# Kernel optimization log

Hardware: AMD Instinct MI355X
Metric: run time of the kernel (lower is better)

The kernel has to match this reference:

```python
import jax, jax.numpy as jnp
import numpy as np

B = 65536
NE = 256   # n_encode
NH = 256   # n_hidden
NC = 4     # n_command
D = 64     # n_depth (BatchNorm channels)
F = 32     # n_features
M = D * (F // 2)  # 1024
EPS = 1e-5


def setup_inputs() -> dict:
    key = jax.random.key(0)
    ks = jax.random.split(key, 8)
    s = 0.05
    return {
        "feature": jax.random.normal(ks[0], (B, NE), jnp.float32),
        "hidden":  jax.random.normal(ks[1], (B, NH), jnp.float32),
        "command": jax.random.normal(ks[2], (B, NC), jnp.float32),
        # linear weights (torch Linear stores [out, in]); xavier-like scale
        "Wq":  jax.random.normal(ks[3], (D, NC), jnp.float32) * s,
        "Wkz": jax.random.normal(ks[4], (M, NE), jnp.float32) * s,
        "Wkh": jax.random.normal(ks[5], (M, NH), jnp.float32) * s,
        "Wvz": jax.random.normal(ks[6], (M, NE), jnp.float32) * s,
        "Wvh": jax.random.normal(ks[7], (M, NH), jnp.float32) * s,
        # BatchNorm1d(64) affine params (normV exists in __init__ but is unused)
        "gammaQ": jnp.ones((D,), jnp.float32),
        "betaQ":  jnp.zeros((D,), jnp.float32),
        "gammaK": jnp.ones((D,), jnp.float32),
        "betaK":  jnp.zeros((D,), jnp.float32),
    }


def reference(feature, hidden, command, Wq, Wkz, Wkh, Wvz, Wvh,
              gammaQ, betaQ, gammaK, betaK):
    # Q projection: [B, D]; BatchNorm1d over batch (training-mode batch stats,
    # biased variance, matching torch).
    Q = command @ Wq.T
    mQ = jnp.mean(Q, axis=0)
    vQ = jnp.mean(jnp.square(Q - mQ), axis=0)
    Qn = (Q - mQ) / jnp.sqrt(vQ + EPS) * gammaQ + betaQ          # [B, D]

    # K: cat([B,M],[B,M]) -> [B, 2M] -> view [B, F, D] -> transpose -> [B, D, F]
    K = jnp.concatenate([feature @ Wkz.T, hidden @ Wkh.T], axis=1)
    K = K.reshape(-1, F, D).transpose(0, 2, 1)                    # [B, D, F]
    mK = jnp.mean(K, axis=(0, 2), keepdims=True)
    vK = jnp.mean(jnp.square(K - mK), axis=(0, 2), keepdims=True)
    Kn = (K - mK) / jnp.sqrt(vK + EPS) * gammaK[None, :, None] + betaK[None, :, None]

    # V: [B, F, D], NOT batch-normed (normV is dead code in the original)
    V = jnp.concatenate([feature @ Wvz.T, hidden @ Wvh.T], axis=1).reshape(-1, F, D)

    # attention: [B,1,D] @ [B,D,F] -> [B,F] scores; softmax over F; then @ V
    A = jax.nn.softmax(jnp.einsum('bd,bdf->bf', Qn, Kn) / np.sqrt(D).astype(np.float32), axis=-1)
    s = jnp.einsum('bf,bfd->bd', A, V)                            # [B, D]
    return s
```

## Files before the change

kernel.cpp:

```cpp
#include <hip/hip_runtime.h>
#include <hip/hip_bf16.h>
#include <math.h>


typedef float  f32x4   __attribute__((ext_vector_type(4)));
typedef float  f32x16  __attribute__((ext_vector_type(16)));
typedef __bf16 bf16x4  __attribute__((ext_vector_type(4)));
typedef __bf16 bf16x8  __attribute__((ext_vector_type(8)));

#define MFMA16(A, B, C) __builtin_amdgcn_mfma_f32_16x16x32_bf16((A), (B), (C), 0, 0, 0)
#define MFMA32(A, B, C) __builtin_amdgcn_mfma_f32_32x32x16_bf16((A), (B), (C), 0, 0, 0)

#define EPSV 1e-5f

#define WS_WV    0x000000u
#define WS_WKF   0x100000u
#define WS_G     0x120000u
#define WS_CS    0x1A0000u
#define WS_CMDP  0x1A0800u
#define WS_T     0x1A1800u
#define WS_U     0x1A3800u
#define WS_WQ2   0x1A5800u
#define WS_C0    0x1A5C00u

__global__ __launch_bounds__(512, 2) void setup1(const float* __restrict__ feat,
        const float* __restrict__ hid, const float4* __restrict__ cmd,
        const float* __restrict__ Wvz, const float* __restrict__ Wvh,
        __bf16* __restrict__ WV, float* __restrict__ CMDP, float* __restrict__ CS,
        __bf16* __restrict__ Gp)
{
    __shared__ __bf16 T[256 * 40];
    __shared__ float sm[8][14];
    const int blk = blockIdx.x;
    const int tid = threadIdx.x;

    if (blk >= 384) {
        const int b2 = blk - 384;
        float v[14];
#pragma unroll
        for (int k = 0; k < 14; ++k) v[k] = 0.f;
#pragma unroll
        for (int i = 0; i < 4; ++i) {
            float4 c = cmd[(b2 * 4 + i) * 512 + tid];
            v[0] += c.x;  v[1] += c.y;  v[2] += c.z;  v[3] += c.w;
            v[4] += c.x*c.x; v[5] += c.x*c.y; v[6] += c.x*c.z; v[7] += c.x*c.w;
            v[8] += c.y*c.y; v[9] += c.y*c.z; v[10] += c.y*c.w;
            v[11] += c.z*c.z; v[12] += c.z*c.w; v[13] += c.w*c.w;
        }
#pragma unroll
        for (int k = 0; k < 14; ++k) {
            float s = v[k];
#pragma unroll
            for (int off = 32; off; off >>= 1) s += __shfl_xor(s, off);
            if ((tid & 63) == 0) sm[tid >> 6][k] = s;
        }
        __syncthreads();
        if (tid < 14) {
            float s = 0.f;
#pragma unroll
            for (int w = 0; w < 8; ++w) s += sm[w][tid];
            CMDP[b2 * 14 + tid] = s;
        }
        return;
    }
    if (blk >= 128) {
        int t = (blk - 128) * 512 + tid;
        int e = t * 4;
        const float* src = (e < 262144) ? (Wvz + e) : (Wvh + (e - 262144));
        float4 a = *(const float4*)src;
        bf16x4 vv = { (__bf16)a.x, (__bf16)a.y, (__bf16)a.z, (__bf16)a.w };
        *(bf16x4*)(WV + e) = vv;
        return;
    }

    const int mat  = blk >> 6;
    const int chunk = blk & 63;
    const float* X = mat ? hid : feat;
    float* cs = CS + mat * 256;
    const int k0   = chunk * 1024;
    const int wid  = tid >> 6, lane = tid & 63, quad = lane >> 4, l15 = lane & 15;
    const int c    = tid & 255;
    const int t8   = tid >> 8;

    f32x4 acc[2][16];
#pragma unroll
    for (int mt = 0; mt < 2; ++mt)
#pragma unroll
        for (int nt = 0; nt < 16; ++nt) acc[mt][nt] = (f32x4){0.f, 0.f, 0.f, 0.f};

    float clsum = 0.f;
    for (int it = 0; it < 32; ++it) {
        __syncthreads();
        const int kb = k0 + it * 32;
#pragma unroll
        for (int i = 0; i < 16; ++i) {
            int k = t8 + 2 * i;
            float x = X[(size_t)(kb + k) * 256 + c];
            clsum += x;
            T[c * 40 + k] = (__bf16)x;
        }
        __syncthreads();
        bf16x8 a0 = *(const bf16x8*)&T[(wid * 32 +      l15) * 40 + quad * 8];
        bf16x8 a1 = *(const bf16x8*)&T[(wid * 32 + 16 + l15) * 40 + quad * 8];
#pragma unroll
        for (int nt = 0; nt < 16; ++nt) {
            bf16x8 b = *(const bf16x8*)&T[(nt * 16 + l15) * 40 + quad * 8];
            acc[0][nt] = MFMA16(a0, b, acc[0][nt]);
            acc[1][nt] = MFMA16(a1, b, acc[1][nt]);
        }
    }
    atomicAdd(&cs[c], clsum);
    __bf16* outp = Gp + (size_t)blk * 65536;
#pragma unroll
    for (int mt = 0; mt < 2; ++mt)
#pragma unroll
        for (int nt = 0; nt < 16; ++nt)
#pragma unroll
            for (int r = 0; r < 4; ++r) {
                int gi = wid * 32 + mt * 16 + quad * 4 + r;
                int gj = nt * 16 + l15;
                outp[gi * 256 + gj] = (__bf16)acc[mt][nt][r];
            }
}

__global__ void gram_reduce(const __bf16* __restrict__ Gp, float* __restrict__ G)
{
    int o = blockIdx.x * 256 + threadIdx.x;
    int mat = o >> 16, e = o & 65535;
    const __bf16* p = Gp + (size_t)mat * 64 * 65536 + e;
    float s = 0.f;
#pragma unroll 8
    for (int c = 0; c < 64; ++c) s += (float)p[(size_t)c * 65536];
    G[o] = s;
}

__global__ void rowstats(const float* __restrict__ Wkz, const float* __restrict__ Wkh,
        const float* __restrict__ G, const float* __restrict__ CS,
        float* __restrict__ Tout, float* __restrict__ Uout)
{
    const int blk = blockIdx.x;
    const int mat = blk >> 7, jg = blk & 127;
    const float* Wsrc = (mat ? Wkh : Wkz) + (size_t)jg * 8 * 256;
    const float* Gm = G + (size_t)mat * 65536;
    const float* cs = CS + mat * 256;
    __shared__ float wlT[256 * 8];
    __shared__ float red[4][16];
    const int tid = threadIdx.x, wid = tid >> 6, lane = tid & 63;
#pragma unroll
    for (int jj = 0; jj < 8; ++jj) wlT[tid * 8 + jj] = Wsrc[jj * 256 + tid];
    __syncthreads();
    float inner[8];
#pragma unroll
    for (int jj = 0; jj < 8; ++jj) inner[jj] = 0.f;
    for (int r = 0; r < 256; ++r) {
        float g = Gm[r * 256 + tid];
        float4 w0 = *(const float4*)&wlT[r * 8];
        float4 w1 = *(const float4*)&wlT[r * 8 + 4];
        inner[0] = fmaf(w0.x, g, inner[0]); inner[1] = fmaf(w0.y, g, inner[1]);
        inner[2] = fmaf(w0.z, g, inner[2]); inner[3] = fmaf(w0.w, g, inner[3]);
        inner[4] = fmaf(w1.x, g, inner[4]); inner[5] = fmaf(w1.y, g, inner[5]);
        inner[6] = fmaf(w1.z, g, inner[6]); inner[7] = fmaf(w1.w, g, inner[7]);
    }
    float cst = cs[tid];
#pragma unroll
    for (int jj = 0; jj < 8; ++jj) {
        float wme = wlT[tid * 8 + jj];
        float p = wme * inner[jj];
        float u = wme * cst;
#pragma unroll
        for (int off = 32; off; off >>= 1) { p += __shfl_xor(p, off); u += __shfl_xor(u, off); }
        if (lane == 0) { red[wid][jj] = p; red[wid][jj + 8] = u; }
    }
    __syncthreads();
    if (tid < 16) {
        float s = red[0][tid] + red[1][tid] + red[2][tid] + red[3][tid];
        int jj = tid & 7;
        int j = mat * 1024 + jg * 8 + jj;
        if (tid < 8) Tout[j] = s; else Uout[j] = s;
    }
}

__global__ void finalize_kernel(const float* __restrict__ Wq,
        const float* __restrict__ gQ, const float* __restrict__ bQ,
        const float* __restrict__ gK, const float* __restrict__ bK,
        const float* __restrict__ CMDP, const float* __restrict__ T,
        const float* __restrict__ U, float* __restrict__ Wq2, float* __restrict__ C0)
{
    __shared__ float s14[14];
    const int d = threadIdx.x;
    if (d < 14) {
        float s = 0.f;
        for (int b = 0; b < 32; ++b) s += CMDP[b * 14 + d];
        s14[d] = s;
    }
    __syncthreads();
    float s4[4] = { s14[0], s14[1], s14[2], s14[3] };
    float gc[4][4];
    gc[0][0] = s14[4];
    gc[0][1] = gc[1][0] = s14[5];
    gc[0][2] = gc[2][0] = s14[6];
    gc[0][3] = gc[3][0] = s14[7];
    gc[1][1] = s14[8];
    gc[1][2] = gc[2][1] = s14[9];
    gc[1][3] = gc[3][1] = s14[10];
    gc[2][2] = s14[11];
    gc[2][3] = gc[3][2] = s14[12];
    gc[3][3] = s14[13];
    float wq[4];
#pragma unroll
    for (int c = 0; c < 4; ++c) wq[c] = Wq[d * 4 + c];
    const float invB = 1.0f / 65536.0f;
    float mQ = (wq[0]*s4[0] + wq[1]*s4[1] + wq[2]*s4[2] + wq[3]*s4[3]) * invB;
    float eq2 = 0.f;
#pragma unroll
    for (int c = 0; c < 4; ++c)
#pragma unroll
        for (int c2 = 0; c2 < 4; ++c2) eq2 += wq[c] * wq[c2] * gc[c][c2];
    eq2 *= invB;
    float vQ  = eq2 - mQ * mQ;
    float aQ  = gQ[d] / sqrtf(vQ + EPSV);
    float bQv = bQ[d] - mQ * aQ;
    float S2 = 0.f, S1 = 0.f;
#pragma unroll
    for (int f = 0; f < 32; ++f) { S2 += T[f * 64 + d]; S1 += U[f * 64 + d]; }
    const float invBF = 1.0f / (65536.0f * 32.0f);
    float e2 = S2 * invBF, mK = S1 * invBF;
    float vK = e2 - mK * mK;
    float aK = gK[d] / sqrtf(vK + EPSV);
    float c1 = aQ * aK * 0.125f;
    C0[d] = bQv * aK * 0.125f;
#pragma unroll
    for (int c = 0; c < 4; ++c) Wq2[d * 4 + c] = c1 * wq[c];
}

__global__ void foldK(const float* __restrict__ Wkz, const float* __restrict__ Wkh,
                      const float* __restrict__ Wq2, const float* __restrict__ C0,
                      __bf16* __restrict__ WKF)
{
    const int blk = blockIdx.x;
    const int h = blk / 96, rr = blk % 96;
    const int k = threadIdx.x;
    float s = 0.f;
    if (rr < 80) {
        const int c = rr >> 4, fl = rr & 15;
        const float* Wsrc = (h ? Wkh : Wkz) + (size_t)fl * 64 * 256;
        for (int d = 0; d < 64; ++d) {
            float coef = (c == 0) ? C0[d] : Wq2[d * 4 + (c - 1)];
            s = fmaf(coef, Wsrc[d * 256 + k], s);
        }
    }
    WKF[(size_t)(h * 96 + rr) * 256 + k] = (__bf16)s;
}

__global__ __launch_bounds__(256, 2) void fused_attn(
        const float* __restrict__ feat, const float* __restrict__ hid,
        const float4* __restrict__ cmd, const __bf16* __restrict__ WV,
        const __bf16* __restrict__ WKF, float* __restrict__ out)
{
    __shared__ __bf16 BUF[32768];
    __shared__ __bf16 WGTs[16 * 128];
    const int tid  = threadIdx.x;
    const int wid  = tid >> 6, lane = tid & 63;
    const int l5   = lane & 31, hi = lane >> 5;
    const int fl   = l5 & 15;
    const bool low = (l5 < 16);
    const int wrow = (blockIdx.x << 7) + (wid << 5);

    float l_i[16];
    f32x16 s_acc[2];
#pragma unroll
    for (int r = 0; r < 16; ++r) { l_i[r] = 0.f; s_acc[0][r] = 0.f; s_acc[1][r] = 0.f; }

    bf16x8 st[8];

    for (int h = 0; h < 2; ++h) {
        const float* X = h ? hid : feat;
        const __bf16* Wkf = WKF + ((size_t)h * 96 << 8);

        bf16x8 a2[16];
#pragma unroll
        for (int u = 0; u < 16; ++u) {
            const float* p = X + ((size_t)(wrow + l5) << 8) + u * 16 + hi * 8;
            float4 x0 = *(const float4*)p;
            float4 x1 = *(const float4*)(p + 4);
            a2[u] = (bf16x8){ (__bf16)x0.x, (__bf16)x0.y, (__bf16)x0.z, (__bf16)x0.w,
                              (__bf16)x1.x, (__bf16)x1.y, (__bf16)x1.z, (__bf16)x1.w };
        }

        __syncthreads();
#pragma unroll
        for (int i = 0; i < 12; ++i) {
            int cc = tid + i * 256;
            int n = cc >> 5, k8 = cc & 31;
            bf16x8 v = *(const bf16x8*)(Wkf + n * 256 + k8 * 8);
            *(bf16x8*)&BUF[n * 256 + ((k8 ^ (n & 7)) << 3)] = v;
        }
        __syncthreads();

        f32x16 acc1[3];
#pragma unroll
        for (int nt = 0; nt < 3; ++nt)
#pragma unroll
            for (int r = 0; r < 16; ++r) acc1[nt][r] = 0.f;
#pragma unroll
        for (int ks = 0; ks < 16; ++ks)
#pragma unroll
            for (int nt = 0; nt < 3; ++nt) {
                int n = nt * 32 + l5;
                bf16x8 b = *(const bf16x8*)&BUF[n * 256 + (((ks * 2 + hi) ^ (n & 7)) << 3)];
                acc1[nt] = MFMA32(a2[ks], b, acc1[nt]);
            }

#pragma unroll
        for (int g = 0; g < 4; ++g) {
            bf16x4 wv4;
#pragma unroll
            for (int j = 0; j < 4; ++j) {
                const int r = g * 4 + j;
                const int row32 = j + 8 * g + 4 * hi;
                float4 cm = cmd[wrow + row32];
                float e0, e1, t0[3], t1[3];
#pragma unroll
                for (int nt = 0; nt < 3; ++nt) {
                    e0 = acc1[nt][r];
                    e1 = __shfl_xor(e0, 16);
                    t0[nt] = low ? e0 : e1;
                    t1[nt] = low ? e1 : e0;
                }
                float sc = t0[0] + cm.x * t1[0] + cm.y * t0[1]
                                 + cm.z * t1[1] + cm.w * t0[2];
                float w = __expf(sc);
                wv4[j] = (__bf16)w;
                float ws = w;
                ws += __shfl_xor(ws, 1); ws += __shfl_xor(ws, 2);
                ws += __shfl_xor(ws, 4); ws += __shfl_xor(ws, 8);
                l_i[r] += ws;
            }
            if (low) *(bf16x4*)&WGTs[fl * 128 + (wid << 5) + 8 * g + 4 * hi] = wv4;
        }

        if (h == 0) {
            const __bf16* base = WV;
#pragma unroll
            for (int i = 0; i < 8; ++i) {
                int cc = tid + i * 256;
                int n = cc >> 5, k8 = cc & 31;
                st[i] = *(const bf16x8*)(base + n * 256 + k8 * 8);
            }
        }
        __syncthreads();

        for (int f2 = 0; f2 < 16; ++f2) {
            const int bufsel = (f2 & 1) << 14;
#pragma unroll
            for (int i = 0; i < 8; ++i) {
                int cc = tid + i * 256;
                int n = cc >> 5, k8 = cc & 31;
                *(bf16x8*)&BUF[bufsel + n * 256 + ((k8 ^ (n & 7)) << 3)] = st[i];
            }
            __syncthreads();
            const int g2 = h * 16 + f2 + 1;
            if (g2 < 32) {
                const __bf16* base = WV + ((size_t)g2 << 14);
#pragma unroll
                for (int i = 0; i < 8; ++i) {
                    int cc = tid + i * 256;
                    int n = cc >> 5, k8 = cc & 31;
                    st[i] = *(const bf16x8*)(base + n * 256 + k8 * 8);
                }
            }
            f32x16 acc2[2];
#pragma unroll
            for (int r = 0; r < 16; ++r) { acc2[0][r] = 0.f; acc2[1][r] = 0.f; }
#pragma unroll
            for (int ks = 0; ks < 16; ++ks)
#pragma unroll
                for (int nt = 0; nt < 2; ++nt) {
                    int n = nt * 32 + l5;
                    bf16x8 b = *(const bf16x8*)&BUF[bufsel + n * 256
                                                    + (((ks * 2 + hi) ^ (n & 7)) << 3)];
                    acc2[nt] = MFMA32(a2[ks], b, acc2[nt]);
                }
#pragma unroll
            for (int g = 0; g < 4; ++g) {
                bf16x4 wv = *(const bf16x4*)&WGTs[f2 * 128 + (wid << 5) + 8 * g + 4 * hi];
#pragma unroll
                for (int j = 0; j < 4; ++j) {
                    float w = (float)wv[j];
                    s_acc[0][g * 4 + j] += w * acc2[0][g * 4 + j];
                    s_acc[1][g * 4 + j] += w * acc2[1][g * 4 + j];
                }
            }
        }
    }

#pragma unroll
    for (int g = 0; g < 4; ++g)
#pragma unroll
        for (int j = 0; j < 4; ++j) {
            const int r = g * 4 + j;
            float inv = 1.0f / l_i[r];
            size_t row = (size_t)(wrow + j + 8 * g + 4 * hi);
            out[(row << 6) + l5]      = s_acc[0][r] * inv;
            out[(row << 6) + 32 + l5] = s_acc[1][r] * inv;
        }
}

extern "C" void kernel_launch(void* const* d_in, const int* in_sizes, int n_in,
                              void* d_out, int out_size, void* d_ws, size_t ws_size,
                              hipStream_t stream)
{
    (void)in_sizes; (void)n_in; (void)out_size; (void)ws_size;
    const float* feature = (const float*)d_in[0];
    const float* hidden  = (const float*)d_in[1];
    const float* command = (const float*)d_in[2];
    const float* Wq      = (const float*)d_in[3];
    const float* Wkz     = (const float*)d_in[4];
    const float* Wkh     = (const float*)d_in[5];
    const float* Wvz     = (const float*)d_in[6];
    const float* Wvh     = (const float*)d_in[7];
    const float* gammaQ  = (const float*)d_in[8];
    const float* betaQ   = (const float*)d_in[9];
    const float* gammaK  = (const float*)d_in[10];
    const float* betaK   = (const float*)d_in[11];

    char* ws = (char*)d_ws;
    __bf16* WV   = (__bf16*)(ws + WS_WV);
    __bf16* WKF  = (__bf16*)(ws + WS_WKF);
    float*  G    = (float*)(ws + WS_G);
    float*  CS   = (float*)(ws + WS_CS);
    float*  CMDP = (float*)(ws + WS_CMDP);
    float*  Tj   = (float*)(ws + WS_T);
    float*  Uj   = (float*)(ws + WS_U);
    float*  Wq2  = (float*)(ws + WS_WQ2);
    float*  C0   = (float*)(ws + WS_C0);
    float*  outp = (float*)d_out;
    __bf16* Gp   = (__bf16*)d_out;

    hipMemsetAsync(ws + WS_CS, 0, 0x800, stream);
    setup1<<<416, 512, 0, stream>>>(feature, hidden, (const float4*)command,
                                    Wvz, Wvh, WV, CMDP, CS, Gp);
    gram_reduce<<<512, 256, 0, stream>>>(Gp, G);
    rowstats<<<256, 256, 0, stream>>>(Wkz, Wkh, G, CS, Tj, Uj);
    finalize_kernel<<<1, 64, 0, stream>>>(Wq, gammaQ, betaQ, gammaK, betaK,
                                          CMDP, Tj, Uj, Wq2, C0);
    foldK<<<192, 256, 0, stream>>>(Wkz, Wkh, Wq2, C0, WKF);
    fused_attn<<<512, 256, 0, stream>>>(feature, hidden, (const float4*)command,
                                        WV, WKF, outp);
}
```

Baseline: 374.0 us.

## Load weight tiles straight into LDS with global_load_lds and raise MFMA priority

The key-weight and value-weight tiles now go from global memory directly into swizzled LDS through the global_load_lds builtin, replacing the register-staged load-then-store path. The value-weight loop keeps two LDS buffers and issues the next tile's asynchronous load right after the barrier, while MFMAs run on the current buffer. This frees the staging VGPRs and removes the LDS store instructions. It also wraps the MFMA loops in s_setprio and adds a sched_barrier. The risk is correctness: it relies on barriers waiting for the DMA loads to finish, and the fixed per-wave lane-to-row mapping must cover every row.

Measured after the change: 360.3 us. 1.04x faster.

```diff
diff --git a/kernel.cpp b/kernel.cpp
--- a/kernel.cpp
+++ b/kernel.cpp
@@ -22,6 +22,13 @@
 #define WS_U     0x1A3800u
 #define WS_WQ2   0x1A5800u
 #define WS_C0    0x1A5C00u
+
+__device__ __forceinline__ void gl_lds16(const void* g, void* l)
+{
+    __builtin_amdgcn_global_load_lds(
+        (const __attribute__((address_space(1))) unsigned int*)g,
+        (__attribute__((address_space(3))) unsigned int*)l, 16, 0, 0);
+}
 
 __global__ __launch_bounds__(512, 2) void setup1(const float* __restrict__ feat,
         const float* __restrict__ hid, const float4* __restrict__ cmd,
@@ -266,12 +273,17 @@
     const bool low = (l5 < 16);
     const int wrow = (blockIdx.x << 7) + (wid << 5);
 
+    int voff[12];
+#pragma unroll
+    for (int i = 0; i < 12; ++i) {
+        int n = (wid << 1) + (i << 3) + hi;
+        voff[i] = n * 256 + ((l5 ^ (n & 7)) << 3);
+    }
+
     float l_i[16];
     f32x16 s_acc[2];
 #pragma unroll
     for (int r = 0; r < 16; ++r) { l_i[r] = 0.f; s_acc[0][r] = 0.f; s_acc[1][r] = 0.f; }
-
-    bf16x8 st[8];
 
     for (int h = 0; h < 2; ++h) {
         const float* X = h ? hid : feat;
@@ -289,12 +301,8 @@
 
         __syncthreads();
 #pragma unroll
-        for (int i = 0; i < 12; ++i) {
-            int cc = tid + i * 256;
-            int n = cc >> 5, k8 = cc & 31;
-            bf16x8 v = *(const bf16x8*)(Wkf + n * 256 + k8 * 8);
-            *(bf16x8*)&BUF[n * 256 + ((k8 ^ (n & 7)) << 3)] = v;
-        }
+        for (int i = 0; i < 12; ++i)
+            gl_lds16(Wkf + voff[i], &BUF[((wid << 1) + (i << 3)) << 8]);
         __syncthreads();
 
         f32x16 acc1[3];
@@ -302,6 +310,7 @@
         for (int nt = 0; nt < 3; ++nt)
 #pragma unroll
             for (int r = 0; r < 16; ++r) acc1[nt][r] = 0.f;
+        __builtin_amdgcn_s_setprio(1);
 #pragma unroll
         for (int ks = 0; ks < 16; ++ks)
 #pragma unroll
@@ -310,6 +319,7 @@
                 bf16x8 b = *(const bf16x8*)&BUF[n * 256 + (((ks * 2 + hi) ^ (n & 7)) << 3)];
                 acc1[nt] = MFMA32(a2[ks], b, acc1[nt]);
             }
+        __builtin_amdgcn_s_setprio(0);
 
 #pragma unroll
         for (int g = 0; g < 4; ++g) {
@@ -339,39 +349,30 @@
             if (low) *(bf16x4*)&WGTs[fl * 128 + (wid << 5) + 8 * g + 4 * hi] = wv4;
         }
 
-        if (h == 0) {
-            const __bf16* base = WV;
-#pragma unroll
-            for (int i = 0; i < 8; ++i) {
-                int cc = tid + i * 256;
-                int n = cc >> 5, k8 = cc & 31;
-                st[i] = *(const bf16x8*)(base + n * 256 + k8 * 8);
-            }
-        }
-        __syncthreads();
+        __syncthreads();
+
+        {
+            const __bf16* base = WV + ((size_t)(h * 16) << 14);
+#pragma unroll
+            for (int i = 0; i < 8; ++i)
+                gl_lds16(base + voff[i], &BUF[((wid << 1) + (i << 3)) << 8]);
+        }
 
         for (int f2 = 0; f2 < 16; ++f2) {
             const int bufsel = (f2 & 1) << 14;
-#pragma unroll
-            for (int i = 0; i < 8; ++i) {
-                int cc = tid + i * 256;
-                int n = cc >> 5, k8 = cc & 31;
-                *(bf16x8*)&BUF[bufsel + n * 256 + ((k8 ^ (n & 7)) << 3)] = st[i];
+            __syncthreads();
+            if (f2 < 15) {
+                const __bf16* base = WV + ((size_t)(h * 16 + f2 + 1) << 14);
+                const int nsel = bufsel ^ 16384;
+#pragma unroll
+                for (int i = 0; i < 8; ++i)
+                    gl_lds16(base + voff[i], &BUF[nsel + ((((wid << 1) + (i << 3))) << 8)]);
             }
-            __syncthreads();
-            const int g2 = h * 16 + f2 + 1;
-            if (g2 < 32) {
-                const __bf16* base = WV + ((size_t)g2 << 14);
-#pragma unroll
-                for (int i = 0; i < 8; ++i) {
-                    int cc = tid + i * 256;
-                    int n = cc >> 5, k8 = cc & 31;
-                    st[i] = *(const bf16x8*)(base + n * 256 + k8 * 8);
-                }
-            }
+            __builtin_amdgcn_sched_barrier(0);
             f32x16 acc2[2];
 #pragma unroll
             for (int r = 0; r < 16; ++r) { acc2[0][r] = 0.f; acc2[1][r] = 0.f; }
+            __builtin_amdgcn_s_setprio(1);
 #pragma unroll
             for (int ks = 0; ks < 16; ++ks)
 #pragma unroll
@@ -381,6 +382,7 @@
                                                     + (((ks * 2 + hi) ^ (n & 7)) << 3)];
                     acc2[nt] = MFMA32(a2[ks], b, acc2[nt]);
                 }
+            __builtin_amdgcn_s_setprio(0);
 #pragma unroll
             for (int g = 0; g < 4; ++g) {
                 bf16x4 wv = *(const bf16x4*)&WGTs[f2 * 128 + (wid << 5) + 8 * g + 4 * hi];
```
